# Kernel tuning notes

Measured on AMD Instinct MI355X. Metric: run time of the kernel, lower is better.

Reference implementation:

```python
import jax, jax.numpy as jnp
import numpy as np

B, T = 32, 1024
AC, SE, H, NH = 20, 16, 64, 4
HD = H // NH  # 16


def setup_inputs() -> dict:
    key = jax.random.key(0)
    ks = jax.random.split(key, 8)
    g = 0.1  # xavier gain used in _init_weights (rough scale)
    return {
        'acoustic': jax.random.normal(ks[0], (B, T, AC), jnp.float32),
        'semantic': jax.random.normal(ks[1], (B, T, SE), jnp.float32),
        'Wq': jax.random.normal(ks[2], (H, SE), jnp.float32) * g,
        'bq': jnp.zeros((H,), jnp.float32),
        'Wkv': jax.random.normal(ks[3], (2 * H, AC), jnp.float32) * g,
        'bkv': jnp.zeros((2 * H,), jnp.float32),
        'in_w': jax.random.normal(ks[4], (3 * H, H), jnp.float32) * g,
        'in_b': jnp.zeros((3 * H,), jnp.float32),
        'out_w': jax.random.normal(ks[5], (H, H), jnp.float32) * g,
        'out_b': jnp.zeros((H,), jnp.float32),
        'proj_w': jax.random.normal(ks[6], (AC, H), jnp.float32) * g,
        'proj_b': jnp.zeros((AC,), jnp.float32),
        'residual_logit': jnp.float32(-2.0),
        'ln_gamma': jnp.ones((AC,), jnp.float32),
        'ln_beta': jnp.zeros((AC,), jnp.float32),
    }


def _std(x, axis, keepdims=True):
    # torch.std default: unbiased (ddof=1)
    return jnp.std(x, axis=axis, ddof=1, keepdims=keepdims)


def reference(acoustic, semantic, Wq, bq, Wkv, bkv, in_w, in_b, out_w, out_b,
              proj_w, proj_b, residual_logit, ln_gamma, ln_beta):
    # projections to hidden space
    q = semantic @ Wq.T + bq                       # [B,T,H]
    kv = acoustic @ Wkv.T + bkv                    # [B,T,2H]
    k, v = kv[..., :H], kv[..., H:]
    # nn.MultiheadAttention in-projection
    qi = q @ in_w[:H].T + in_b[:H]
    ki = k @ in_w[H:2 * H].T + in_b[H:2 * H]
    vi = v @ in_w[2 * H:].T + in_b[2 * H:]
    # split heads -> [B,T,NH,HD]
    qh = qi.reshape(B, T, NH, HD)
    kh = ki.reshape(B, T, NH, HD)
    vh = vi.reshape(B, T, NH, HD)
    scores = jnp.einsum('bqhd,bkhd->bhqk', qh, kh) / jnp.sqrt(jnp.float32(HD))
    attn = jax.nn.softmax(scores, axis=-1)         # [B,NH,T,T]
    ctx = jnp.einsum('bhqk,bkhd->bqhd', attn, vh).reshape(B, T, H)
    attended = ctx @ out_w.T + out_b               # MHA out_proj
    enhanced_raw = attended @ proj_w.T + proj_b    # [B,T,AC]
    enhanced = acoustic + jax.nn.sigmoid(residual_logit) * enhanced_raw

    # statistics over batch+time (no_grad in torch -> stop_gradient)
    orig_mean = jax.lax.stop_gradient(jnp.mean(acoustic, axis=(0, 1), keepdims=True))
    orig_std = jax.lax.stop_gradient(_std(acoustic, (0, 1)) + 1e-8)
    a_n = (acoustic - orig_mean) / orig_std
    e_n = (enhanced - orig_mean) / orig_std
    std_ratio = _std(e_n, (0, 1)) / (_std(a_n, (0, 1)) + 1e-8)
    std_corr = jnp.where(std_ratio < 0.4, 0.4 / std_ratio, jnp.ones_like(std_ratio))
    enhanced_final = (e_n * std_corr) * orig_std + orig_mean

    # LayerNorm over last dim (biased variance, eps=1e-5)
    mu = jnp.mean(enhanced_final, axis=-1, keepdims=True)
    var = jnp.mean(jnp.square(enhanced_final - mu), axis=-1, keepdims=True)
    return (enhanced_final - mu) * jax.lax.rsqrt(var + 1e-5) * ln_gamma + ln_beta
```

## Files before the change

### kernel.cpp

```cpp
#include <hip/hip_runtime.h>
#include <hip/hip_bf16.h>
#include <math.h>

#define B 32
#define T 1024
#define AC 20
#define SE 16
#define H 64
#define NH 4
#define HD 16
#define NROW (B*T)
#define BH (B*NH)
#define NCHUNK (T/32)
#define NSLOT 128

typedef unsigned short u16;
typedef short short8 __attribute__((ext_vector_type(8)));
typedef float f32x16 __attribute__((ext_vector_type(16)));
typedef unsigned int uintx4 __attribute__((ext_vector_type(4)));

#define F_KB   (BH*T*16/2)
#define F_VT   (BH*32768/2)
#define OFF_KB   0
#define OFF_VT   (OFF_KB + F_KB)
#define OFF_ET   (OFF_VT + F_VT)
#define OFF_WF   (OFF_ET + AC*NROW)
#define OFF_ACC  (OFF_WF + 5120)
#define OFF_ST   (OFF_ACC + NSLOT*80)

#define WF_WQ 0
#define WF_BQ 1024
#define WF_WK 1088
#define WF_BK 2368
#define WF_WV 2432
#define WF_BV 3712
#define WF_WO 3776
#define WF_BO 5056
#define WF_TOTAL 5076

#define QSCALE 0.36067375670234045f

__device__ __forceinline__ u16 bf16b(float a) {
    __hip_bfloat16 t = __float2bfloat16(a);
    u16 u; __builtin_memcpy(&u, &t, 2); return u;
}
__device__ __forceinline__ unsigned packbf(float a, float b) {
    return (unsigned)bf16b(a) | ((unsigned)bf16b(b) << 16);
}

__global__ __launch_bounds__(256) void k_fuse(
    const float* __restrict__ Wq, const float* __restrict__ bq,
    const float* __restrict__ Wkv, const float* __restrict__ bkv,
    const float* __restrict__ in_w, const float* __restrict__ in_b,
    const float* __restrict__ out_w, const float* __restrict__ out_b,
    const float* __restrict__ proj_w, const float* __restrict__ proj_b,
    float* __restrict__ wf, float* __restrict__ accum) {
    int idx = blockIdx.x * 256 + threadIdx.x;
    if (idx < NSLOT*40) {
        accum[idx] = 0.f;
        accum[idx + NSLOT*40] = 0.f;
    }
    if (idx >= WF_TOTAL) return;
    if (idx < WF_BQ) {
        int i = idx >> 4, j = idx & 15;
        float s = 0.f;
        for (int m = 0; m < H; ++m) s += in_w[i*H + m] * Wq[m*SE + j];
        wf[idx] = QSCALE * s;
    } else if (idx < WF_WK) {
        int i = idx - WF_BQ;
        float s = in_b[i];
        for (int m = 0; m < H; ++m) s += in_w[i*H + m] * bq[m];
        wf[idx] = QSCALE * s;
    } else if (idx < WF_BK) {
        int r = idx - WF_WK; int i = r / AC, j = r % AC;
        float s = 0.f;
        for (int m = 0; m < H; ++m) s += in_w[(H+i)*H + m] * Wkv[m*AC + j];
        wf[idx] = s;
    } else if (idx < WF_WV) {
        int i = idx - WF_BK;
        float s = in_b[H + i];
        for (int m = 0; m < H; ++m) s += in_w[(H+i)*H + m] * bkv[m];
        wf[idx] = s;
    } else if (idx < WF_BV) {
        int r = idx - WF_WV; int i = r / AC, j = r % AC;
        float s = 0.f;
        for (int m = 0; m < H; ++m) s += in_w[(2*H+i)*H + m] * Wkv[(H+m)*AC + j];
        wf[idx] = s;
    } else if (idx < WF_WO) {
        int i = idx - WF_BV;
        float s = in_b[2*H + i];
        for (int m = 0; m < H; ++m) s += in_w[(2*H+i)*H + m] * bkv[H + m];
        wf[idx] = s;
    } else if (idx < WF_BO) {
        int r = idx - WF_WO; int c = r >> 6, d = r & 63;
        float s = 0.f;
        for (int m = 0; m < H; ++m) s += proj_w[c*H + m] * out_w[m*H + d];
        wf[idx] = s;
    } else {
        int c = idx - WF_BO;
        float s = proj_b[c];
        for (int m = 0; m < H; ++m) s += proj_w[c*H + m] * out_b[m];
        wf[idx] = s;
    }
}

__global__ __launch_bounds__(128) void k_qkv(
    const float* __restrict__ acst, const float* __restrict__ wf,
    u16* __restrict__ Kb, u16* __restrict__ Vtb) {
    __shared__ __align__(16) unsigned vls32[16*33];
    const int tid = threadIdx.x;
    const int sec = tid >> 4, r = tid & 15;
    const int row = blockIdx.x * 16 + r;
    const int b = row >> 10, t = row & 1023;
    const int type = sec >> 2, h = sec & 3;
    float o[16];
    {
        float a[AC];
        const float4* ap = (const float4*)(acst + (size_t)row * AC);
        #pragma unroll
        for (int i = 0; i < 5; ++i) {
            float4 v = ap[i];
            a[4*i] = v.x; a[4*i+1] = v.y; a[4*i+2] = v.z; a[4*i+3] = v.w;
        }
        const float* wb = wf + (type == 0 ? WF_WK : WF_WV) + h*16*AC;
        const float* bb = wf + (type == 0 ? WF_BK : WF_BV) + h*16;
        #pragma unroll
        for (int ii = 0; ii < 16; ++ii) {
            float acc = bb[ii];
            #pragma unroll
            for (int j = 0; j < 5; ++j) {
                float4 w4 = *(const float4*)(wb + ii*AC + 4*j);
                acc += a[4*j]*w4.x + a[4*j+1]*w4.y + a[4*j+2]*w4.z + a[4*j+3]*w4.w;
            }
            o[ii] = acc;
        }
    }
    if (type == 0) {
        unsigned* dst = (unsigned*)(Kb + (((size_t)(b*NH + h))*T + t)*16);
        #pragma unroll
        for (int i = 0; i < 8; ++i) dst[i] = packbf(o[2*i], o[2*i+1]);
    } else {
        u16* v16 = (u16*)vls32;
        #pragma unroll
        for (int d = 0; d < HD; ++d) v16[d*66 + h*16 + r] = bf16b(o[d]);
    }
    __syncthreads();
    if (type == 1) {
        const int l = tid - 64, h2 = l >> 4, li = l & 15;
        const int bb_ = blockIdx.x >> 6, g = blockIdx.x & 63;
        const size_t tile = (size_t)((bb_*NH + h2)*64 + g);
        unsigned tmp[8];
        #pragma unroll
        for (int k = 0; k < 8; ++k) tmp[k] = vls32[li*33 + h2*8 + k];
        unsigned* dst = (unsigned*)(Vtb + tile*512) + li*8;
        *(uintx4*)dst       = (uintx4){tmp[0], tmp[1], tmp[2], tmp[3]};
        *(uintx4*)(dst + 4) = (uintx4){tmp[4], tmp[5], tmp[6], tmp[7]};
        if (li == 0) {
            unsigned* od = (unsigned*)(Vtb + tile*512 + 256);
            const unsigned one2 = 0x3F803F80u;
            *(uintx4*)od       = (uintx4){one2, one2, one2, one2};
            *(uintx4*)(od + 4) = (uintx4){one2, one2, one2, one2};
        }
    }
}

#define CSTR 66
__global__ __launch_bounds__(256, 4) void k_attn(
    const float* __restrict__ sem,
    const u16* __restrict__ Kb, const u16* __restrict__ Vtb,
    const float* __restrict__ acst, const float* __restrict__ wf,
    const float* __restrict__ rlogit,
    float* __restrict__ enhT, float* __restrict__ accum) {
    __shared__ __align__(16) float ctxs[32*CSTR];
    __shared__ __align__(16) float wsm[AC*H + AC];
    __shared__ __align__(16) float wqs[16*H + H];
    const int tid  = threadIdx.x;
    const int lane = tid & 63;
    const int wv   = tid >> 6;
    for (int i = tid; i < AC*H + AC; i += 256) wsm[i] = wf[WF_WO + i];
    for (int i = tid; i < 16*H + H; i += 256) wqs[i] = wf[WF_WQ + i];
    const int blk  = blockIdx.x;
    const int b    = blk & 31;
    const int qblk = blk >> 5;
    const int l31 = lane & 31, hi2 = lane >> 5;
    const int bh = b*NH + wv;
    const int q0 = qblk*32;
    __syncthreads();

    short8 qf;
    {
        float s[SE];
        const float4* sp = (const float4*)(sem + ((size_t)b*T + q0 + l31) * SE);
        #pragma unroll
        for (int i = 0; i < 4; ++i) {
            float4 v = sp[i];
            s[4*i] = v.x; s[4*i+1] = v.y; s[4*i+2] = v.z; s[4*i+3] = v.w;
        }
        #pragma unroll
        for (int jj = 0; jj < 8; ++jj) {
            const int ii = wv*16 + hi2*8 + jj;
            float acc0 = wqs[1024 + ii];
            #pragma unroll
            for (int j = 0; j < 4; ++j) {
                float4 w4 = *(const float4*)(wqs + ii*SE + 4*j);
                acc0 += s[4*j]*w4.x + s[4*j+1]*w4.y + s[4*j+2]*w4.z + s[4*j+3]*w4.w;
            }
            qf[jj] = (short)bf16b(acc0);
        }
    }

    const u16* kp = Kb + ((size_t)bh*T + l31)*16 + 8*hi2;
    const u16* vp = Vtb + (size_t)bh*32768 + l31*16 + 8*hi2;

    f32x16 acc = {0.f,0.f,0.f,0.f,0.f,0.f,0.f,0.f,0.f,0.f,0.f,0.f,0.f,0.f,0.f,0.f};
    const f32x16 z16 = {0.f,0.f,0.f,0.f,0.f,0.f,0.f,0.f,0.f,0.f,0.f,0.f,0.f,0.f,0.f,0.f};

    auto chunk = [&](short8 kf, short8 va, short8 vb) {
        f32x16 sc = __builtin_amdgcn_mfma_f32_32x32x16_bf16(kf, qf, z16, 0, 0, 0);
        float p[16];
        #pragma unroll
        for (int r = 0; r < 16; ++r) p[r] = __builtin_amdgcn_exp2f(sc[r]);
        unsigned u0, u1, u2, u3, u4, u5, u6, u7;
        asm("v_cvt_pk_bf16_f32 %0, %1, %2" : "=v"(u0) : "v"(p[0]),  "v"(p[1]));
        asm("v_cvt_pk_bf16_f32 %0, %1, %2" : "=v"(u1) : "v"(p[2]),  "v"(p[3]));
        asm("v_cvt_pk_bf16_f32 %0, %1, %2" : "=v"(u2) : "v"(p[4]),  "v"(p[5]));
        asm("v_cvt_pk_bf16_f32 %0, %1, %2" : "=v"(u3) : "v"(p[6]),  "v"(p[7]));
        asm("v_cvt_pk_bf16_f32 %0, %1, %2" : "=v"(u4) : "v"(p[8]),  "v"(p[9]));
        asm("v_cvt_pk_bf16_f32 %0, %1, %2" : "=v"(u5) : "v"(p[10]), "v"(p[11]));
        asm("v_cvt_pk_bf16_f32 %0, %1, %2" : "=v"(u6) : "v"(p[12]), "v"(p[13]));
        asm("v_cvt_pk_bf16_f32 %0, %1, %2" : "=v"(u7) : "v"(p[14]), "v"(p[15]));
        asm("v_permlane32_swap_b32 %0, %1" : "+v"(u2), "+v"(u0));
        asm("v_permlane32_swap_b32 %0, %1" : "+v"(u3), "+v"(u1));
        asm("v_permlane32_swap_b32 %0, %1" : "+v"(u6), "+v"(u4));
        asm("v_permlane32_swap_b32 %0, %1" : "+v"(u7), "+v"(u5));
        uintx4 t1 = {u0, u1, u2, u3};
        uintx4 t2 = {u4, u5, u6, u7};
        short8 pf1 = __builtin_bit_cast(short8, t1);
        short8 pf2 = __builtin_bit_cast(short8, t2);
        acc = __builtin_amdgcn_mfma_f32_32x32x16_bf16(va, pf1, acc, 0, 0, 0);
        acc = __builtin_amdgcn_mfma_f32_32x32x16_bf16(vb, pf2, acc, 0, 0, 0);
    };

    short8 kfA = *(const short8*)kp;
    short8 vaA = *(const short8*)vp;
    short8 vbA = *(const short8*)(vp + 512);
    short8 kfB = *(const short8*)(kp + 512);
    short8 vaB = *(const short8*)(vp + 1024);
    short8 vbB = *(const short8*)(vp + 1536);
    for (int ch = 0; ch < NCHUNK; ch += 2) {
        const int n0 = (ch + 2 < NCHUNK) ? ch + 2 : ch;
        short8 kfN0 = *(const short8*)(kp + (size_t)n0*512);
        short8 vaN0 = *(const short8*)(vp + (size_t)n0*1024);
        short8 vbN0 = *(const short8*)(vp + (size_t)n0*1024 + 512);
        chunk(kfA, vaA, vbA);
        const int n1 = (ch + 3 < NCHUNK) ? ch + 3 : ch + 1;
        short8 kfN1 = *(const short8*)(kp + (size_t)n1*512);
        short8 vaN1 = *(const short8*)(vp + (size_t)n1*1024);
        short8 vbN1 = *(const short8*)(vp + (size_t)n1*1024 + 512);
        chunk(kfB, vaB, vbB);
        kfA = kfN0; vaA = vaN0; vbA = vbN0;
        kfB = kfN1; vaB = vaN1; vbB = vbN1;
    }

    const float ls = __shfl(acc[8], l31);
    const float inv = 1.f / ls;
    #pragma unroll
    for (int r = 0; r < 8; ++r) {
        const int d = (r & 3) + 8*(r >> 2) + 4*hi2;
        ctxs[l31*CSTR + wv*16 + d] = acc[r] * inv;
    }
    __syncthreads();

    const int rq = tid & 31, g = tid >> 5;
    const int row = b*T + q0 + rq;
    const float sg = 1.f / (1.f + __expf(-rlogit[0]));
    float* slot = accum + (size_t)(blk & (NSLOT-1)) * 80;
    const int nj = (g < 4) ? 3 : 2;
    for (int j = 0; j < nj; ++j) {
        const int ch = g + 8*j;
        float s = wsm[AC*H + ch];
        #pragma unroll
        for (int kc = 0; kc < 4; ++kc) {
            float c0 = ctxs[rq*CSTR + kc*16 +  0], c1 = ctxs[rq*CSTR + kc*16 +  1];
            float c2 = ctxs[rq*CSTR + kc*16 +  2], c3 = ctxs[rq*CSTR + kc*16 +  3];
            float c4 = ctxs[rq*CSTR + kc*16 +  4], c5 = ctxs[rq*CSTR + kc*16 +  5];
            float c6 = ctxs[rq*CSTR + kc*16 +  6], c7 = ctxs[rq*CSTR + kc*16 +  7];
            float c8 = ctxs[rq*CSTR + kc*16 +  8], c9 = ctxs[rq*CSTR + kc*16 +  9];
            float cA = ctxs[rq*CSTR + kc*16 + 10], cB = ctxs[rq*CSTR + kc*16 + 11];
            float cC = ctxs[rq*CSTR + kc*16 + 12], cD = ctxs[rq*CSTR + kc*16 + 13];
            float cE = ctxs[rq*CSTR + kc*16 + 14], cF = ctxs[rq*CSTR + kc*16 + 15];
            const float* w = wsm + ch*H + kc*16;
            s += c0*w[0] + c1*w[1] + c2*w[2] + c3*w[3]
               + c4*w[4] + c5*w[5] + c6*w[6] + c7*w[7]
               + c8*w[8] + c9*w[9] + cA*w[10] + cB*w[11]
               + cC*w[12] + cD*w[13] + cE*w[14] + cF*w[15];
        }
        const float a = acst[(size_t)row*AC + ch];
        const float e = a + sg * s;
        enhT[(size_t)ch * NROW + row] = e;
        float sa = a, qa = a*a, se = e, qe = e*e;
        #pragma unroll
        for (int m = 1; m <= 16; m <<= 1) {
            sa += __shfl_xor(sa, m); qa += __shfl_xor(qa, m);
            se += __shfl_xor(se, m); qe += __shfl_xor(qe, m);
        }
        if (rq == 0) {
            atomicAdd(&slot[ch*4+0], sa);
            atomicAdd(&slot[ch*4+1], qa);
            atomicAdd(&slot[ch*4+2], se);
            atomicAdd(&slot[ch*4+3], qe);
        }
    }
}

__global__ __launch_bounds__(640) void k_stats2(
    const float* __restrict__ accum, float* __restrict__ stats) {
    __shared__ float red[80*8];
    __shared__ float acs[80];
    const int tx = threadIdx.x;
    const int c = tx >> 3, p = tx & 7;
    float s0 = 0.f, s1 = 0.f, s2 = 0.f, s3 = 0.f;
    #pragma unroll
    for (int i = 0; i < 4; ++i) {
        int sl = p + (4*i)*8;
        s0 += accum[(size_t)sl*80 + c];
        s1 += accum[(size_t)(sl+8)*80 + c];
        s2 += accum[(size_t)(sl+16)*80 + c];
        s3 += accum[(size_t)(sl+24)*80 + c];
    }
    red[c*8 + p] = (s0 + s1) + (s2 + s3);
    __syncthreads();
    if (tx < 80) {
        float t = 0.f;
        #pragma unroll
        for (int i = 0; i < 8; ++i) t += red[tx*8 + i];
        acs[tx] = t;
    }
    __syncthreads();
    if (tx < AC) {
        const float Nf = (float)NROW;
        float sa = acs[tx*4+0], qa = acs[tx*4+1];
        float se = acs[tx*4+2], qe = acs[tx*4+3];
        float mu  = sa / Nf;
        float va  = (qa - sa*sa/Nf) / (Nf - 1.f);
        float sda = sqrtf(fmaxf(va, 0.f));
        float osd = sda + 1e-8f;
        float ve  = (qe - se*se/Nf) / (Nf - 1.f);
        float sde = sqrtf(fmaxf(ve, 0.f));
        float ratio = (sde / osd) / (sda / osd + 1e-8f);
        float corr  = (ratio < 0.4f) ? (0.4f / ratio) : 1.f;
        stats[tx*2]   = mu;
        stats[tx*2+1] = corr;
    }
}

__global__ __launch_bounds__(128) void k_final(
    const float* __restrict__ enhT, const float* __restrict__ stats,
    const float* __restrict__ gamma, const float* __restrict__ beta,
    float* __restrict__ out) {
    __shared__ float acs[40];
    const int tx = threadIdx.x;
    if (tx < 40) acs[tx] = stats[tx];
    __syncthreads();
    int row = blockIdx.x * 128 + tx;
    float ef[AC];
    #pragma unroll
    for (int c = 0; c < AC; ++c) {
        float mu = acs[c*2], corr = acs[c*2+1];
        float e = enhT[(size_t)c * NROW + row];
        ef[c] = (e - mu) * corr + mu;
    }
    float m = 0.f;
    #pragma unroll
    for (int c = 0; c < AC; ++c) m += ef[c];
    m *= (1.f / AC);
    float v = 0.f;
    #pragma unroll
    for (int c = 0; c < AC; ++c) { float d = ef[c] - m; v += d*d; }
    v *= (1.f / AC);
    float inv = rsqrtf(v + 1e-5f);
    float o[AC];
    #pragma unroll
    for (int c = 0; c < AC; ++c) o[c] = (ef[c] - m) * inv * gamma[c] + beta[c];
    float4* op = (float4*)(out + (size_t)row * AC);
    #pragma unroll
    for (int i = 0; i < 5; ++i)
        op[i] = make_float4(o[4*i], o[4*i+1], o[4*i+2], o[4*i+3]);
}

extern "C" void kernel_launch(void* const* d_in, const int* in_sizes, int n_in,
                              void* d_out, int out_size, void* d_ws, size_t ws_size,
                              hipStream_t stream) {
    (void)in_sizes; (void)n_in; (void)out_size; (void)ws_size;
    const float* acoustic = (const float*)d_in[0];
    const float* semantic = (const float*)d_in[1];
    const float* Wq     = (const float*)d_in[2];
    const float* bq     = (const float*)d_in[3];
    const float* Wkv    = (const float*)d_in[4];
    const float* bkv    = (const float*)d_in[5];
    const float* in_w   = (const float*)d_in[6];
    const float* in_b   = (const float*)d_in[7];
    const float* out_w  = (const float*)d_in[8];
    const float* out_b  = (const float*)d_in[9];
    const float* proj_w = (const float*)d_in[10];
    const float* proj_b = (const float*)d_in[11];
    const float* rlogit = (const float*)d_in[12];
    const float* gamma  = (const float*)d_in[13];
    const float* beta   = (const float*)d_in[14];
    float* ws = (float*)d_ws;
    u16* Kb  = (u16*)(ws + OFF_KB);
    u16* Vtb = (u16*)(ws + OFF_VT);
    float* enhT  = ws + OFF_ET;
    float* wf    = ws + OFF_WF;
    float* accum = ws + OFF_ACC;
    float* stats = ws + OFF_ST;
    float* out = (float*)d_out;

    k_fuse<<<(WF_TOTAL + 255)/256, 256, 0, stream>>>(Wq, bq, Wkv, bkv, in_w, in_b,
                                                     out_w, out_b, proj_w, proj_b, wf, accum);
    k_qkv<<<NROW/16, 128, 0, stream>>>(acoustic, wf, Kb, Vtb);
    k_attn<<<1024, 256, 0, stream>>>(semantic, Kb, Vtb, acoustic, wf, rlogit, enhT, accum);
    k_stats2<<<1, 640, 0, stream>>>(accum, stats);
    k_final<<<NROW/128, 128, 0, stream>>>(enhT, stats, gamma, beta, out);
}
```

Baseline: 139.7 us.

## Split attention key range across two wave halves per head and merge in LDS

The attention block doubles to 512 threads so each head gets two waves, each processing half of the key sequence (16 chunks instead of 32). Partial unnormalized contexts and row sums are written to two shared buffers, then summed and normalized before the output projection. This shortens the serial per-wave MFMA/exp loop and raises wave-level parallelism, at the cost of extra LDS traffic, an additional barrier, and higher occupancy demands (launch bounds 512,8 may constrain registers). Weight staging into LDS is also vectorized to float4.

```diff
diff --git a/kernel.cpp b/kernel.cpp
--- a/kernel.cpp
+++ b/kernel.cpp
@@ -11,7 +11,7 @@
 #define HD 16
 #define NROW (B*T)
 #define BH (B*NH)
-#define NCHUNK (T/32)
+#define NCH2 16
 #define NSLOT 128
 
 typedef unsigned short u16;
@@ -165,25 +165,34 @@
 }
 
 #define CSTR 66
-__global__ __launch_bounds__(256, 4) void k_attn(
+__global__ __launch_bounds__(512, 8) void k_attn(
     const float* __restrict__ sem,
     const u16* __restrict__ Kb, const u16* __restrict__ Vtb,
     const float* __restrict__ acst, const float* __restrict__ wf,
     const float* __restrict__ rlogit,
     float* __restrict__ enhT, float* __restrict__ accum) {
-    __shared__ __align__(16) float ctxs[32*CSTR];
+    __shared__ __align__(16) float ctxA[32*CSTR];
+    __shared__ __align__(16) float ctxB[32*CSTR];
     __shared__ __align__(16) float wsm[AC*H + AC];
     __shared__ __align__(16) float wqs[16*H + H];
+    __shared__ float lsl[8*32];
     const int tid  = threadIdx.x;
     const int lane = tid & 63;
     const int wv   = tid >> 6;
-    for (int i = tid; i < AC*H + AC; i += 256) wsm[i] = wf[WF_WO + i];
-    for (int i = tid; i < 16*H + H; i += 256) wqs[i] = wf[WF_WQ + i];
+    const int h    = wv & 3, khalf = wv >> 2;
+    {
+        const float4* s4 = (const float4*)(wf + WF_WO);
+        float4* d4 = (float4*)wsm;
+        for (int i = tid; i < 325; i += 512) d4[i] = s4[i];
+        const float4* q4 = (const float4*)(wf + WF_WQ);
+        float4* e4 = (float4*)wqs;
+        for (int i = tid; i < 272; i += 512) e4[i] = q4[i];
+    }
     const int blk  = blockIdx.x;
     const int b    = blk & 31;
     const int qblk = blk >> 5;
     const int l31 = lane & 31, hi2 = lane >> 5;
-    const int bh = b*NH + wv;
+    const int bh = b*NH + h;
     const int q0 = qblk*32;
     __syncthreads();
 
@@ -198,7 +207,7 @@
         }
         #pragma unroll
         for (int jj = 0; jj < 8; ++jj) {
-            const int ii = wv*16 + hi2*8 + jj;
+            const int ii = h*16 + hi2*8 + jj;
             float acc0 = wqs[1024 + ii];
             #pragma unroll
             for (int j = 0; j < 4; ++j) {
@@ -209,8 +218,8 @@
         }
     }
 
-    const u16* kp = Kb + ((size_t)bh*T + l31)*16 + 8*hi2;
-    const u16* vp = Vtb + (size_t)bh*32768 + l31*16 + 8*hi2;
+    const u16* kp = Kb + ((size_t)bh*T + khalf*512 + l31)*16 + 8*hi2;
+    const u16* vp = Vtb + (size_t)bh*32768 + (size_t)khalf*16384 + l31*16 + 8*hi2;
 
     f32x16 acc = {0.f,0.f,0.f,0.f,0.f,0.f,0.f,0.f,0.f,0.f,0.f,0.f,0.f,0.f,0.f,0.f};
     const f32x16 z16 = {0.f,0.f,0.f,0.f,0.f,0.f,0.f,0.f,0.f,0.f,0.f,0.f,0.f,0.f,0.f,0.f};
@@ -247,13 +256,13 @@
     short8 kfB = *(const short8*)(kp + 512);
     short8 vaB = *(const short8*)(vp + 1024);
     short8 vbB = *(const short8*)(vp + 1536);
-    for (int ch = 0; ch < NCHUNK; ch += 2) {
-        const int n0 = (ch + 2 < NCHUNK) ? ch + 2 : ch;
+    for (int ch = 0; ch < NCH2; ch += 2) {
+        const int n0 = (ch + 2 < NCH2) ? ch + 2 : ch;
         short8 kfN0 = *(const short8*)(kp + (size_t)n0*512);
         short8 vaN0 = *(const short8*)(vp + (size_t)n0*1024);
         short8 vbN0 = *(const short8*)(vp + (size_t)n0*1024 + 512);
         chunk(kfA, vaA, vbA);
-        const int n1 = (ch + 3 < NCHUNK) ? ch + 3 : ch + 1;
+        const int n1 = (ch + 3 < NCH2) ? ch + 3 : ch + 1;
         short8 kfN1 = *(const short8*)(kp + (size_t)n1*512);
         short8 vaN1 = *(const short8*)(vp + (size_t)n1*1024);
         short8 vbN1 = *(const short8*)(vp + (size_t)n1*1024 + 512);
@@ -262,12 +271,25 @@
         kfB = kfN1; vaB = vaN1; vbB = vbN1;
     }
 
-    const float ls = __shfl(acc[8], l31);
-    const float inv = 1.f / ls;
+    float* ctxH = (khalf == 0) ? ctxA : ctxB;
     #pragma unroll
     for (int r = 0; r < 8; ++r) {
         const int d = (r & 3) + 8*(r >> 2) + 4*hi2;
-        ctxs[l31*CSTR + wv*16 + d] = acc[r] * inv;
+        ctxH[l31*CSTR + h*16 + d] = acc[r];
+    }
+    if (hi2 == 0) lsl[wv*32 + l31] = acc[8];
+    __syncthreads();
+
+    {
+        const int rq2 = tid >> 4;
+        const int k0 = (tid & 15) * 4;
+        const int hh = k0 >> 4;
+        const float inv2 = 1.f / (lsl[hh*32 + rq2] + lsl[(4+hh)*32 + rq2]);
+        #pragma unroll
+        for (int k = 0; k < 4; ++k) {
+            const int ix = rq2*CSTR + k0 + k;
+            ctxA[ix] = (ctxA[ix] + ctxB[ix]) * inv2;
+        }
     }
     __syncthreads();
 
@@ -275,20 +297,20 @@
     const int row = b*T + q0 + rq;
     const float sg = 1.f / (1.f + __expf(-rlogit[0]));
     float* slot = accum + (size_t)(blk & (NSLOT-1)) * 80;
-    const int nj = (g < 4) ? 3 : 2;
+    const int nj = (g < 4) ? 2 : 1;
     for (int j = 0; j < nj; ++j) {
-        const int ch = g + 8*j;
+        const int ch = g + 16*j;
         float s = wsm[AC*H + ch];
         #pragma unroll
         for (int kc = 0; kc < 4; ++kc) {
-            float c0 = ctxs[rq*CSTR + kc*16 +  0], c1 = ctxs[rq*CSTR + kc*16 +  1];
-            float c2 = ctxs[rq*CSTR + kc*16 +  2], c3 = ctxs[rq*CSTR + kc*16 +  3];
-            float c4 = ctxs[rq*CSTR + kc*16 +  4], c5 = ctxs[rq*CSTR + kc*16 +  5];
-            float c6 = ctxs[rq*CSTR + kc*16 +  6], c7 = ctxs[rq*CSTR + kc*16 +  7];
-            float c8 = ctxs[rq*CSTR + kc*16 +  8], c9 = ctxs[rq*CSTR + kc*16 +  9];
-            float cA = ctxs[rq*CSTR + kc*16 + 10], cB = ctxs[rq*CSTR + kc*16 + 11];
-            float cC = ctxs[rq*CSTR + kc*16 + 12], cD = ctxs[rq*CSTR + kc*16 + 13];
-            float cE = ctxs[rq*CSTR + kc*16 + 14], cF = ctxs[rq*CSTR + kc*16 + 15];
+            float c0 = ctxA[rq*CSTR + kc*16 +  0], c1 = ctxA[rq*CSTR + kc*16 +  1];
+            float c2 = ctxA[rq*CSTR + kc*16 +  2], c3 = ctxA[rq*CSTR + kc*16 +  3];
+            float c4 = ctxA[rq*CSTR + kc*16 +  4], c5 = ctxA[rq*CSTR + kc*16 +  5];
+            float c6 = ctxA[rq*CSTR + kc*16 +  6], c7 = ctxA[rq*CSTR + kc*16 +  7];
+            float c8 = ctxA[rq*CSTR + kc*16 +  8], c9 = ctxA[rq*CSTR + kc*16 +  9];
+            float cA = ctxA[rq*CSTR + kc*16 + 10], cB = ctxA[rq*CSTR + kc*16 + 11];
+            float cC = ctxA[rq*CSTR + kc*16 + 12], cD = ctxA[rq*CSTR + kc*16 + 13];
+            float cE = ctxA[rq*CSTR + kc*16 + 14], cF = ctxA[rq*CSTR + kc*16 + 15];
             const float* w = wsm + ch*H + kc*16;
             s += c0*w[0] + c1*w[1] + c2*w[2] + c3*w[3]
                + c4*w[4] + c5*w[5] + c6*w[6] + c7*w[7]
@@ -419,7 +441,7 @@
     k_fuse<<<(WF_TOTAL + 255)/256, 256, 0, stream>>>(Wq, bq, Wkv, bkv, in_w, in_b,
                                                      out_w, out_b, proj_w, proj_b, wf, accum);
     k_qkv<<<NROW/16, 128, 0, stream>>>(acoustic, wf, Kb, Vtb);
-    k_attn<<<1024, 256, 0, stream>>>(semantic, Kb, Vtb, acoustic, wf, rlogit, enhT, accum);
+    k_attn<<<1024, 512, 0, stream>>>(semantic, Kb, Vtb, acoustic, wf, rlogit, enhT, accum);
     k_stats2<<<1, 640, 0, stream>>>(accum, stats);
     k_final<<<NROW/128, 128, 0, stream>>>(enhT, stats, gamma, beta, out);
 }
```

Measured after the change: 184.0 us. 1.32x slower.
